# Performance work log

Hardware: AMD Instinct MI355X
Metric: run time of the kernel (lower is better)

The kernel has to match this reference:

```python
import jax, jax.numpy as jnp
import numpy as np

B, CL, TT, D, A, L, G, H = 8, 2048, 1024, 768, 320, 6, 8192, 12
F = 4 * D


def setup_inputs():
    ks = iter(jax.random.split(jax.random.key(0), 80))

    def nrm(shape, std=1.0):
        return jax.random.normal(next(ks), shape, jnp.float32) * std

    sD, sA, sF = 1.0 / np.sqrt(D), 1.0 / np.sqrt(A), 1.0 / np.sqrt(F)
    inp = {
        'context_latents': nrm((B, CL, D)),
        'action_latents': nrm((B, A)),
        'target_indices': jax.random.randint(next(ks), (B, TT), 0, G),
        'ad_w1': nrm((A, D), sA), 'ad_b1': jnp.zeros(D),
        'ad_lnw': jnp.ones(D), 'ad_lnb': jnp.zeros(D),
        'ad_w2': nrm((D, D), sD), 'ad_b2': jnp.zeros(D),
        'mq': nrm((G, D), sD),
        'ln1_w': jnp.ones((L, D)), 'ln1_b': jnp.zeros((L, D)),
        'a_qw': nrm((L, D, D), sD), 'a_qb': jnp.zeros((L, D)),
        'a_kw': nrm((L, D, D), sD), 'a_kb': jnp.zeros((L, D)),
        'a_vw': nrm((L, D, D), sD), 'a_vb': jnp.zeros((L, D)),
        'a_cw': nrm((L, D, D), sD), 'a_cb': jnp.zeros((L, D)),
        'ln2_w': jnp.ones((L, D)), 'ln2_b': jnp.zeros((L, D)),
        's_qw': nrm((L, D, D), sD), 's_qb': jnp.zeros((L, D)),
        's_kw': nrm((L, D, D), sD), 's_kb': jnp.zeros((L, D)),
        's_vw': nrm((L, D, D), sD), 's_vb': jnp.zeros((L, D)),
        's_cw': nrm((L, D, D), sD), 's_cb': jnp.zeros((L, D)),
        'ln3_w': jnp.ones((L, D)), 'ln3_b': jnp.zeros((L, D)),
        'mlp_w1': nrm((L, D, F), sD), 'mlp_b1': jnp.zeros((L, F)),
        'mlp_w2': nrm((L, F, D), sF), 'mlp_b2': jnp.zeros((L, D)),
        'fn_w': jnp.ones(D), 'fn_b': jnp.zeros(D),
        'mu_w': nrm((D, D), sD), 'mu_b': jnp.zeros(D),
        'lv_w': nrm((D, D), sD), 'lv_b': jnp.zeros(D),
    }
    return inp


def _ln(x, w, b, eps=1e-5):
    m = x.mean(-1, keepdims=True)
    v = jnp.var(x, axis=-1, keepdims=True)
    return (x - m) * jax.lax.rsqrt(v + eps) * w + b


def _lin_attn(x, kv, qw, qb, kw, kb, vw, vb, cw, cb):
    # BioLinearAttention: elu(x)+1 feature map, k^T@v reformulation (O(T*hd^2))
    Bq, Tq, Dm = x.shape
    Tk = kv.shape[1]
    hd = Dm // H
    q = (x @ qw + qb).reshape(Bq, Tq, H, hd).transpose(0, 2, 1, 3)
    k = (kv @ kw + kb).reshape(Bq, Tk, H, hd).transpose(0, 2, 1, 3)
    v = (kv @ vw + vb).reshape(Bq, Tk, H, hd).transpose(0, 2, 1, 3)
    q = jax.nn.elu(q) + 1.0
    k = jax.nn.elu(k) + 1.0
    kvm = jnp.einsum('bhkd,bhke->bhde', k, v)  # [B,H,hd,hd]
    ksum = k.sum(axis=2)                        # [B,H,hd]
    z = 1.0 / (jnp.einsum('bhqd,bhd->bhq', q, ksum) + 1e-6)
    y = jnp.einsum('bhqd,bhde->bhqe', q, kvm) * z[..., None]
    y = y.transpose(0, 2, 1, 3).reshape(Bq, Tq, Dm)
    return y @ cw + cb


def reference(context_latents, action_latents, target_indices, ad_w1, ad_b1,
              ad_lnw, ad_lnb, ad_w2, ad_b2, mq, ln1_w, ln1_b, a_qw, a_qb,
              a_kw, a_kb, a_vw, a_vb, a_cw, a_cb, ln2_w, ln2_b, s_qw, s_qb,
              s_kw, s_kb, s_vw, s_vb, s_cw, s_cb, ln3_w, ln3_b, mlp_w1,
              mlp_b1, mlp_w2, mlp_b2, fn_w, fn_b, mu_w, mu_b, lv_w, lv_b):
    # adapter: Linear -> LayerNorm -> GELU(exact) -> Linear
    a = action_latents @ ad_w1 + ad_b1
    a = jax.nn.gelu(_ln(a, ad_lnw, ad_lnb), approximate=False)
    action_emb = (a @ ad_w2 + ad_b2)[:, None, :]  # [B,1,D]
    queries = mq[target_indices]                  # [B,TT,D]
    x = jnp.concatenate([context_latents, queries], axis=1)  # [B,CL+TT,D]
    for i in range(L):
        x = x + _lin_attn(_ln(x, ln1_w[i], ln1_b[i]), action_emb,
                          a_qw[i], a_qb[i], a_kw[i], a_kb[i],
                          a_vw[i], a_vb[i], a_cw[i], a_cb[i])
        xn = _ln(x, ln2_w[i], ln2_b[i])
        x = x + _lin_attn(xn, xn, s_qw[i], s_qb[i], s_kw[i], s_kb[i],
                          s_vw[i], s_vb[i], s_cw[i], s_cb[i])
        h = jax.nn.gelu(_ln(x, ln3_w[i], ln3_b[i]) @ mlp_w1[i] + mlp_b1[i],
                        approximate=True)
        x = x + h @ mlp_w2[i] + mlp_b2[i]
    x = _ln(x, fn_w, fn_b)
    pred = x[:, CL:, :]
    mu = pred @ mu_w + mu_b
    logvar = jnp.clip(pred @ lv_w + lv_b, -10.0, 2.0)
    return mu, logvar
```

## Files before the change

### kernel.cpp

```cpp
#include <hip/hip_runtime.h>
#include <hip/hip_bf16.h>
#include <math.h>

#define B_   8
#define CL_  2048
#define TT_  1024
#define T_   3072
#define D_   768
#define AD_  320
#define L_   6
#define H_   12
#define F_   3072
#define HD_  64
#define BH_  (B_*H_)
#define BT_  (B_*T_)

typedef __bf16 bf16x8 __attribute__((ext_vector_type(8)));
typedef float  f32x4  __attribute__((ext_vector_type(4)));

__device__ __forceinline__ float bf2f(ushort h){
  union { unsigned u; float f; } v; v.u = ((unsigned)h) << 16; return v.f;
}
__device__ __forceinline__ ushort f2bf(float f){
  union { float f; unsigned u; } v; v.f = f;
  unsigned u = v.u;
  return (ushort)((u + 0x7fffu + ((u >> 16) & 1u)) >> 16);
}

__device__ __forceinline__ void gl_lds16(const ushort* g, ushort* l){
  __builtin_amdgcn_global_load_lds((__attribute__((address_space(1))) void*)g,
                                   (__attribute__((address_space(3))) void*)l,
                                   16, 0, 0);
}

__global__ __launch_bounds__(256)
void zero_k(float4* __restrict__ p, int n4)
{
  int i = blockIdx.x*256 + threadIdx.x;
  if (i < n4) p[i] = (float4){0.f,0.f,0.f,0.f};
}

__global__ __launch_bounds__(256)
void tconv_k(const float* __restrict__ in, ushort* __restrict__ out, int K, int N)
{
  __shared__ ushort tile[64*65];
  int n0 = blockIdx.x*64, k0 = blockIdx.y*64;
  int c  = threadIdx.x & 63, rb = threadIdx.x >> 6;
  #pragma unroll
  for (int i = 0; i < 16; i++){
    int r = rb + i*4;
    tile[r*65 + c] = f2bf(in[(size_t)(k0 + r)*N + n0 + c]);
  }
  __syncthreads();
  #pragma unroll
  for (int i = 0; i < 16; i++){
    int r = rb + i*4;
    out[(size_t)(n0 + r)*K + k0 + c] = tile[c*65 + r];
  }
}

template<int EPI>
__global__ __launch_bounds__(256)
void gemm_bf16_k(const ushort* __restrict__ Ag, const ushort* __restrict__ Bt,
                 const float* __restrict__ bias, ushort* __restrict__ outb,
                 float* __restrict__ outf, int N, int K, int lda, int ldb)
{
  __shared__ __align__(16) ushort As[128*64];
  __shared__ __align__(16) ushort Bs[128*64];
  const int tid  = threadIdx.x;
  const int wave = tid >> 6, lane = tid & 63;
  const int q    = lane >> 4, l16 = lane & 15;
  const int bm   = blockIdx.y * 128, bn = blockIdx.x * 128;
  const int wm   = (wave & 1) * 64,  wn = (wave >> 1) * 64;
  const int lr   = lane >> 3;
  const int lc   = ((lane & 7) ^ lr) * 8;

  f32x4 acc[4][4];
  #pragma unroll
  for (int i = 0; i < 4; i++)
    #pragma unroll
    for (int j = 0; j < 4; j++) acc[i][j] = (f32x4){0.f,0.f,0.f,0.f};

  for (int k0 = 0; k0 < K; k0 += 64){
    #pragma unroll
    for (int j = 0; j < 4; j++){
      int r0 = wave*8 + j*32;
      gl_lds16(Ag + (size_t)(bm + r0 + lr)*lda + k0 + lc, As + r0*64);
      gl_lds16(Bt + (size_t)(bn + r0 + lr)*ldb + k0 + lc, Bs + r0*64);
    }
    __syncthreads();
    #pragma unroll
    for (int ks = 0; ks < 2; ks++){
      const int sx = (((ks*4 + q) ^ (l16 & 7)) * 8);
      bf16x8 af[4], bfr[4];
      #pragma unroll
      for (int mt = 0; mt < 4; mt++)
        af[mt]  = *(const bf16x8*)(As + (wm + mt*16 + l16)*64 + sx);
      #pragma unroll
      for (int nt = 0; nt < 4; nt++)
        bfr[nt] = *(const bf16x8*)(Bs + (wn + nt*16 + l16)*64 + sx);
      #pragma unroll
      for (int mt = 0; mt < 4; mt++)
        #pragma unroll
        for (int nt = 0; nt < 4; nt++)
          acc[mt][nt] = __builtin_amdgcn_mfma_f32_16x16x32_bf16(af[mt], bfr[nt], acc[mt][nt], 0, 0, 0);
    }
    __syncthreads();
  }

  #pragma unroll
  for (int nt = 0; nt < 4; nt++){
    int col  = bn + wn + nt*16 + l16;
    float bv = bias ? bias[col] : 0.f;
    #pragma unroll
    for (int mt = 0; mt < 4; mt++){
      #pragma unroll
      for (int r = 0; r < 4; r++){
        int row   = bm + wm + mt*16 + q*4 + r;
        float v   = acc[mt][nt][r] + bv;
        size_t off = (size_t)row*N + col;
        if      (EPI == 0) outb[off] = f2bf(v);
        else if (EPI == 1) outb[off] = f2bf(v > 0.f ? v + 1.f : __expf(v));
        else if (EPI == 2){
          float t = __expf(1.5957691216057308f*v + 0.0713548162726009f*v*v*v);
          outb[off] = f2bf(v - v/(t + 1.f));
        }
        else if (EPI == 3) outf[off] += v;
        else if (EPI == 4) outf[off] = v;
        else if (EPI == 5) outf[off] = fminf(fmaxf(v, -10.f), 2.f);
      }
    }
  }
}

__global__ __launch_bounds__(256)
void y_mfma_k(const ushort* __restrict__ qb, const float* __restrict__ kvm,
              const float* __restrict__ ksum, ushort* __restrict__ yb)
{
  __shared__ __align__(16) ushort Qs[128*72];
  __shared__ __align__(16) ushort Bs[80*72];
  int bh = blockIdx.x, b = bh / H_, h = bh - b*H_;
  int bm = blockIdx.y * 128;
  int tid = threadIdx.x, wave = tid >> 6, lane = tid & 63;
  int q = lane >> 4, l16 = lane & 15;

  const float* kvg = kvm + (size_t)bh*4096;
  #pragma unroll
  for (int rep = 0; rep < 16; rep++){
    int idx = rep*256 + tid;
    int d = idx >> 6, e = idx & 63;
    Bs[e*72 + d] = f2bf(kvg[idx]);
  }
  if (tid < 64) Bs[64*72 + tid] = f2bf(ksum[bh*64 + tid]);
  for (int idx = tid; idx < 15*64; idx += 256){
    int r = 65 + idx/64, c = idx & 63;
    Bs[r*72 + c] = 0;
  }
  const size_t qbase = ((size_t)b*T_ + bm)*D_ + h*HD_;
  #pragma unroll
  for (int i = 0; i < 4; i++){
    int e = i*256 + tid;
    int r = e >> 3, c = (e & 7)*8;
    *(bf16x8*)(Qs + r*72 + c) = *(const bf16x8*)(qb + qbase + (size_t)r*D_ + c);
  }
  __syncthreads();

  int wm = wave*32;
  f32x4 acc[2][5];
  #pragma unroll
  for (int i = 0; i < 2; i++)
    #pragma unroll
    for (int j = 0; j < 5; j++) acc[i][j] = (f32x4){0.f,0.f,0.f,0.f};

  #pragma unroll
  for (int ks = 0; ks < 2; ks++){
    bf16x8 af[2], bfr[5];
    #pragma unroll
    for (int mt = 0; mt < 2; mt++)
      af[mt]  = *(const bf16x8*)(Qs + (wm + mt*16 + l16)*72 + ks*32 + q*8);
    #pragma unroll
    for (int nt = 0; nt < 5; nt++)
      bfr[nt] = *(const bf16x8*)(Bs + (nt*16 + l16)*72 + ks*32 + q*8);
    #pragma unroll
    for (int mt = 0; mt < 2; mt++)
      #pragma unroll
      for (int nt = 0; nt < 5; nt++)
        acc[mt][nt] = __builtin_amdgcn_mfma_f32_16x16x32_bf16(af[mt], bfr[nt], acc[mt][nt], 0, 0, 0);
  }

  #pragma unroll
  for (int mt = 0; mt < 2; mt++){
    #pragma unroll
    for (int r = 0; r < 4; r++){
      float d0 = __shfl(acc[mt][4][r], lane & 48);
      float z  = 1.f / (d0 + 1e-6f);
      int row  = bm + wm + mt*16 + q*4 + r;
      size_t obase = ((size_t)b*T_ + row)*D_ + h*HD_;
      #pragma unroll
      for (int nt = 0; nt < 4; nt++)
        yb[obase + nt*16 + l16] = f2bf(acc[mt][nt][r] * z);
    }
  }
}

__global__ __launch_bounds__(256)
void ln_add_k(float* __restrict__ x, const float* __restrict__ cb,
              const float* __restrict__ w, const float* __restrict__ b,
              ushort* __restrict__ out)
{
  int wave = threadIdx.x >> 6, lane = threadIdx.x & 63;
  int row  = blockIdx.x*4 + wave;
  int bidx = row / T_;
  float* xr = x + (size_t)row*D_;
  const float* cbr = cb + (size_t)bidx*D_;
  float vals[12], s = 0.f, s2 = 0.f;
  #pragma unroll
  for (int j = 0; j < 12; j++){
    int e = j*64 + lane;
    float v = xr[e] + cbr[e];
    xr[e] = v;
    vals[j] = v; s += v; s2 += v*v;
  }
  #pragma unroll
  for (int o = 32; o > 0; o >>= 1){ s += __shfl_xor(s, o); s2 += __shfl_xor(s2, o); }
  float m   = s  * (1.f/768.f);
  float var = s2 * (1.f/768.f) - m*m;
  float rs  = rsqrtf(var + 1e-5f);
  ushort* orow = out + (size_t)row*D_;
  #pragma unroll
  for (int j = 0; j < 12; j++){
    int e = j*64 + lane;
    orow[e] = f2bf((vals[j] - m)*rs*w[e] + b[e]);
  }
}

template<int TAIL>
__global__ __launch_bounds__(256)
void ln_k(const float* __restrict__ x, const float* __restrict__ w,
          const float* __restrict__ b, ushort* __restrict__ out)
{
  int wave = threadIdx.x >> 6, lane = threadIdx.x & 63;
  int row  = blockIdx.x*4 + wave;
  size_t prow;
  if (TAIL){ int bb = row >> 10, t = row & 1023; prow = (size_t)bb*T_ + CL_ + t; }
  else     { prow = row; }
  const float* xr = x + prow*D_;
  float vals[12], s = 0.f, s2 = 0.f;
  #pragma unroll
  for (int j = 0; j < 12; j++){
    float v = xr[j*64 + lane]; vals[j] = v; s += v; s2 += v*v;
  }
  #pragma unroll
  for (int o = 32; o > 0; o >>= 1){ s += __shfl_xor(s, o); s2 += __shfl_xor(s2, o); }
  float m  = s  * (1.f/768.f);
  float var = s2 * (1.f/768.f) - m*m;
  float rs = rsqrtf(var + 1e-5f);
  ushort* orow = out + (size_t)row*D_;
  #pragma unroll
  for (int j = 0; j < 12; j++){
    int e = j*64 + lane;
    orow[e] = f2bf((vals[j] - m)*rs*w[e] + b[e]);
  }
}

__global__ __launch_bounds__(256)
void kvm_k(const ushort* __restrict__ kb, const ushort* __restrict__ vb,
           float* __restrict__ kvm, float* __restrict__ ksum)
{
  __shared__ ushort Ks[32*64], Vs[32*64];
  int bh = blockIdx.x, slice = blockIdx.y;
  int b  = bh / H_, h = bh - b*H_;
  int tid = threadIdx.x;
  int e = tid & 63, dbase = (tid >> 6) * 16;
  float acc[16];
  #pragma unroll
  for (int i = 0; i < 16; i++) acc[i] = 0.f;
  float ksacc = 0.f;
  int r = tid >> 3, c = (tid & 7) * 8;
  const size_t base = (size_t)b*T_*D_ + h*HD_;
  for (int t0 = slice*384; t0 < slice*384 + 384; t0 += 32){
    *(bf16x8*)(Ks + r*64 + c) = *(const bf16x8*)(kb + base + (size_t)(t0 + r)*D_ + c);
    *(bf16x8*)(Vs + r*64 + c) = *(const bf16x8*)(vb + base + (size_t)(t0 + r)*D_ + c);
    __syncthreads();
    #pragma unroll 8
    for (int j = 0; j < 32; j++){
      float vv = bf2f(Vs[j*64 + e]);
      #pragma unroll
      for (int d = 0; d < 16; d++) acc[d] += bf2f(Ks[j*64 + dbase + d]) * vv;
    }
    if (tid < 64){
      #pragma unroll 8
      for (int j = 0; j < 32; j++) ksacc += bf2f(Ks[j*64 + tid]);
    }
    __syncthreads();
  }
  float* kv = kvm + (size_t)bh*4096;
  #pragma unroll
  for (int d = 0; d < 16; d++) atomicAdd(&kv[(dbase + d)*64 + e], acc[d]);
  if (tid < 64) atomicAdd(&ksum[bh*64 + tid], ksacc);
}

__global__ __launch_bounds__(256)
void build_x_k(const float* __restrict__ ctx, const float* __restrict__ mq,
               const int* __restrict__ tgt, float* __restrict__ x)
{
  int idx = blockIdx.x*256 + threadIdx.x;
  int c  = idx % 192;
  int bt = idx / 192;
  int t  = bt % T_, b = bt / T_;
  float4 v;
  if (t < CL_) v = ((const float4*)ctx)[((size_t)b*CL_ + t)*192 + c];
  else {
    int g = tgt[b*TT_ + (t - CL_)];
    v = ((const float4*)mq)[(size_t)g*192 + c];
  }
  ((float4*)x)[idx] = v;
}

__global__ __launch_bounds__(256)
void act1_k(const float* __restrict__ act, const float* __restrict__ w1,
            const float* __restrict__ b1, const float* __restrict__ lnw,
            const float* __restrict__ lnb, float* __restrict__ a1)
{
  __shared__ float buf[768];
  __shared__ float red[256];
  int b = blockIdx.x, tid = threadIdx.x;
  const float* ar = act + b*AD_;
  for (int j = tid; j < 768; j += 256){
    float s = b1[j];
    for (int k = 0; k < AD_; k++) s += ar[k]*w1[k*768 + j];
    buf[j] = s;
  }
  __syncthreads();
  red[tid] = buf[tid] + buf[tid+256] + buf[tid+512];
  __syncthreads();
  for (int o = 128; o > 0; o >>= 1){ if (tid < o) red[tid] += red[tid+o]; __syncthreads(); }
  float m = red[0]*(1.f/768.f);
  __syncthreads();
  float v0 = buf[tid]-m, v1 = buf[tid+256]-m, v2 = buf[tid+512]-m;
  red[tid] = v0*v0 + v1*v1 + v2*v2;
  __syncthreads();
  for (int o = 128; o > 0; o >>= 1){ if (tid < o) red[tid] += red[tid+o]; __syncthreads(); }
  float rs = rsqrtf(red[0]*(1.f/768.f) + 1e-5f);
  __syncthreads();
  for (int j = tid; j < 768; j += 256){
    float v = (buf[j]-m)*rs*lnw[j] + lnb[j];
    a1[b*768 + j] = 0.5f*v*(1.f + erff(v*0.70710678118654752f));
  }
}

__global__ __launch_bounds__(256)
void act2_k(const float* __restrict__ a1, const float* __restrict__ w2,
            const float* __restrict__ b2, float* __restrict__ emb)
{
  __shared__ float inb[768];
  int b = blockIdx.x, tid = threadIdx.x;
  for (int j = tid; j < 768; j += 256) inb[j] = a1[b*768 + j];
  __syncthreads();
  for (int j = tid; j < 768; j += 256){
    float s = b2[j];
    for (int k = 0; k < 768; k++) s += inb[k]*w2[k*768 + j];
    emb[b*768 + j] = s;
  }
}

__global__ __launch_bounds__(256)
void cross_k(const float* __restrict__ emb, const float* __restrict__ vw,
             const float* __restrict__ vbias, const float* __restrict__ cw,
             const float* __restrict__ cbias_in, float* __restrict__ cb_out)
{
  __shared__ float inb[768], tmp[768];
  int b = blockIdx.x, l = blockIdx.y, tid = threadIdx.x;
  const float* wv = vw + (size_t)l*768*768;
  const float* wc = cw + (size_t)l*768*768;
  for (int j = tid; j < 768; j += 256) inb[j] = emb[b*768 + j];
  __syncthreads();
  for (int j = tid; j < 768; j += 256){
    float s = vbias[l*768 + j];
    for (int k = 0; k < 768; k++) s += inb[k]*wv[k*768 + j];
    tmp[j] = s;
  }
  __syncthreads();
  for (int j = tid; j < 768; j += 256){
    float s = cbias_in[l*768 + j];
    for (int k = 0; k < 768; k++) s += tmp[k]*wc[k*768 + j];
    cb_out[((size_t)l*B_ + b)*768 + j] = s;
  }
}

extern "C" void kernel_launch(void* const* d_in, const int* in_sizes, int n_in,
                              void* d_out, int out_size, void* d_ws, size_t ws_size,
                              hipStream_t stream)
{
  (void)in_sizes; (void)n_in; (void)out_size;
  const float* ctx    = (const float*)d_in[0];
  const float* act    = (const float*)d_in[1];
  const int*   tgt    = (const int*)  d_in[2];
  const float* ad_w1  = (const float*)d_in[3];
  const float* ad_b1  = (const float*)d_in[4];
  const float* ad_lnw = (const float*)d_in[5];
  const float* ad_lnb = (const float*)d_in[6];
  const float* ad_w2  = (const float*)d_in[7];
  const float* ad_b2  = (const float*)d_in[8];
  const float* mq     = (const float*)d_in[9];
  const float* a_vw   = (const float*)d_in[16];
  const float* a_vb   = (const float*)d_in[17];
  const float* a_cw   = (const float*)d_in[18];
  const float* a_cb   = (const float*)d_in[19];
  const float* ln2_w  = (const float*)d_in[20];
  const float* ln2_b  = (const float*)d_in[21];
  const float* s_qw   = (const float*)d_in[22];
  const float* s_qb   = (const float*)d_in[23];
  const float* s_kw   = (const float*)d_in[24];
  const float* s_kb   = (const float*)d_in[25];
  const float* s_vw   = (const float*)d_in[26];
  const float* s_vb   = (const float*)d_in[27];
  const float* s_cw   = (const float*)d_in[28];
  const float* s_cb   = (const float*)d_in[29];
  const float* ln3_w  = (const float*)d_in[30];
  const float* ln3_b  = (const float*)d_in[31];
  const float* mlp_w1 = (const float*)d_in[32];
  const float* mlp_b1 = (const float*)d_in[33];
  const float* mlp_w2 = (const float*)d_in[34];
  const float* mlp_b2 = (const float*)d_in[35];
  const float* fn_w   = (const float*)d_in[36];
  const float* fn_b   = (const float*)d_in[37];
  const float* mu_w   = (const float*)d_in[38];
  const float* mu_b   = (const float*)d_in[39];
  const float* lv_w   = (const float*)d_in[40];
  const float* lv_b   = (const float*)d_in[41];

  char* ws = (char*)d_ws;
  size_t off = 0;
  auto alloc = [&](size_t bytes) -> char* {
    char* p = ws + off; off += (bytes + 255) & ~(size_t)255; return p;
  };
  const size_t NTOK = (size_t)BT_;
  float*  x    = (float*) alloc(NTOK*D_*4);
  ushort* xn   = (ushort*)alloc(NTOK*D_*2);
  char*   un   = alloc(3*NTOK*D_*2);
  ushort* qb   = (ushort*)un;
  ushort* kb   = qb + NTOK*D_;
  ushort* vb   = kb + NTOK*D_;
  ushort* hb   = (ushort*)un;
  ushort* wl_sq = (ushort*)alloc((size_t)D_*D_*2);
  ushort* wl_sk = (ushort*)alloc((size_t)D_*D_*2);
  ushort* wl_sv = (ushort*)alloc((size_t)D_*D_*2);
  ushort* wl_sc = (ushort*)alloc((size_t)D_*D_*2);
  ushort* wl_m1 = (ushort*)alloc((size_t)D_*F_*2);
  ushort* wl_m2 = (ushort*)alloc((size_t)F_*D_*2);
  ushort* wt_mu = (ushort*)alloc((size_t)D_*D_*2);
  ushort* wt_lv = (ushort*)alloc((size_t)D_*D_*2);
  float*  kvm   = (float*) alloc((size_t)BH_*HD_*HD_*4);
  float*  ksum  = (float*) alloc((size_t)BH_*HD_*4);
  float*  cbias = (float*) alloc((size_t)L_*B_*D_*4);
  float*  a1    = (float*) alloc((size_t)B_*D_*4);
  float*  emb   = (float*) alloc((size_t)B_*D_*4);

  if (off > ws_size) return;

  dim3 blk(256);

  tconv_k<<<dim3(12,12), blk, 0, stream>>>(mu_w, wt_mu, D_, D_);
  tconv_k<<<dim3(12,12), blk, 0, stream>>>(lv_w, wt_lv, D_, D_);

  act1_k<<<B_, blk, 0, stream>>>(act, ad_w1, ad_b1, ad_lnw, ad_lnb, a1);
  act2_k<<<B_, blk, 0, stream>>>(a1, ad_w2, ad_b2, emb);
  cross_k<<<dim3(B_, L_), blk, 0, stream>>>(emb, a_vw, a_vb, a_cw, a_cb, cbias);

  build_x_k<<<(BT_*192)/256, blk, 0, stream>>>(ctx, mq, tgt, x);

  const int GY = BT_/128;
  const int NZ4 = (BH_*HD_*HD_ + BH_*HD_) / 4;
  for (int i = 0; i < L_; i++){
    tconv_k<<<dim3(12,12), blk, 0, stream>>>(s_qw   + (size_t)i*D_*D_, wl_sq, D_, D_);
    tconv_k<<<dim3(12,12), blk, 0, stream>>>(s_kw   + (size_t)i*D_*D_, wl_sk, D_, D_);
    tconv_k<<<dim3(12,12), blk, 0, stream>>>(s_vw   + (size_t)i*D_*D_, wl_sv, D_, D_);
    tconv_k<<<dim3(12,12), blk, 0, stream>>>(s_cw   + (size_t)i*D_*D_, wl_sc, D_, D_);
    tconv_k<<<dim3(48,12), blk, 0, stream>>>(mlp_w1 + (size_t)i*D_*F_, wl_m1, D_, F_);
    tconv_k<<<dim3(12,48), blk, 0, stream>>>(mlp_w2 + (size_t)i*F_*D_, wl_m2, F_, D_);

    ln_add_k<<<BT_/4, blk, 0, stream>>>(x, cbias + (size_t)i*B_*D_,
                                        ln2_w + i*D_, ln2_b + i*D_, xn);

    gemm_bf16_k<1><<<dim3(6, GY), blk, 0, stream>>>(xn, wl_sq, s_qb + i*D_, qb, nullptr, D_, D_, D_, D_);
    gemm_bf16_k<1><<<dim3(6, GY), blk, 0, stream>>>(xn, wl_sk, s_kb + i*D_, kb, nullptr, D_, D_, D_, D_);
    gemm_bf16_k<0><<<dim3(6, GY), blk, 0, stream>>>(xn, wl_sv, s_vb + i*D_, vb, nullptr, D_, D_, D_, D_);

    zero_k<<<(NZ4 + 255)/256, blk, 0, stream>>>((float4*)kvm, NZ4);
    kvm_k<<<dim3(BH_, 8), blk, 0, stream>>>(kb, vb, kvm, ksum);
    y_mfma_k<<<dim3(BH_, T_/128), blk, 0, stream>>>(qb, kvm, ksum, qb);

    gemm_bf16_k<3><<<dim3(6, GY), blk, 0, stream>>>(qb, wl_sc, s_cb + i*D_, nullptr, x, D_, D_, D_, D_);

    ln_k<0><<<BT_/4, blk, 0, stream>>>(x, ln3_w + i*D_, ln3_b + i*D_, xn);
    for (int c = 0; c < 2; c++){
      gemm_bf16_k<2><<<dim3(12, GY), blk, 0, stream>>>(
          xn, wl_m1 + (size_t)c*1536*D_, mlp_b1 + (size_t)i*F_ + c*1536,
          hb, nullptr, 1536, D_, D_, D_);
      gemm_bf16_k<3><<<dim3(6, GY), blk, 0, stream>>>(
          hb, wl_m2 + (size_t)c*1536, (c == 0) ? (mlp_b2 + (size_t)i*D_) : nullptr,
          nullptr, x, D_, 1536, 1536, F_);
    }
  }

  ln_k<1><<<(B_*TT_)/4, blk, 0, stream>>>(x, fn_w, fn_b, xn);

  float* outmu = (float*)d_out;
  float* outlv = outmu + (size_t)B_*TT_*D_;
  gemm_bf16_k<4><<<dim3(6, (B_*TT_)/128), blk, 0, stream>>>(xn, wt_mu, mu_b, nullptr, outmu, D_, D_, D_, D_);
  gemm_bf16_k<5><<<dim3(6, (B_*TT_)/128), blk, 0, stream>>>(xn, wt_lv, lv_b, nullptr, outlv, D_, D_, D_, D_);
}
```

Baseline: 5.696 ms.

## Batch weight transposes, fuse QKV and mu/logvar GEMMs, split MLP by rows

Merges the four attention-weight transposes into one launch and the two MLP-weight transposes into another. Q, K and V become a single GEMM with N=2304 and a segment-aware epilogue, and the mu and logvar heads become one GEMM. The MLP is now split into two row halves with full F instead of two F-column halves, so W2 is applied once per half with no second accumulate pass. The serial cross-attention constant computation is replaced by parallel atomic-add matvec kernels. These changes reduce launch count and increase per-launch parallelism, but rely on the wl_* and mu/lv weight buffers being contiguous and add atomics and branchy epilogues.

```diff
diff --git a/kernel.cpp b/kernel.cpp
--- a/kernel.cpp
+++ b/kernel.cpp
@@ -40,11 +40,10 @@
   if (i < n4) p[i] = (float4){0.f,0.f,0.f,0.f};
 }
 
-__global__ __launch_bounds__(256)
-void tconv_k(const float* __restrict__ in, ushort* __restrict__ out, int K, int N)
+__device__ __forceinline__ void tconv_body(const float* in, ushort* out,
+                                           int K, int N, int k0, int n0)
 {
   __shared__ ushort tile[64*65];
-  int n0 = blockIdx.x*64, k0 = blockIdx.y*64;
   int c  = threadIdx.x & 63, rb = threadIdx.x >> 6;
   #pragma unroll
   for (int i = 0; i < 16; i++){
@@ -59,10 +58,37 @@
   }
 }
 
+__global__ __launch_bounds__(256)
+void tconv_k(const float* __restrict__ in, ushort* __restrict__ out, int K, int N)
+{
+  tconv_body(in, out, K, N, blockIdx.y*64, blockIdx.x*64);
+}
+
+__global__ __launch_bounds__(256)
+void tconv4_k(const float* __restrict__ s0, const float* __restrict__ s1,
+              const float* __restrict__ s2, const float* __restrict__ s3,
+              ushort* __restrict__ out)
+{
+  int z = blockIdx.z;
+  const float* in = (z == 0) ? s0 : (z == 1) ? s1 : (z == 2) ? s2 : s3;
+  tconv_body(in, out + (size_t)z*D_*D_, D_, D_, blockIdx.y*64, blockIdx.x*64);
+}
+
+__global__ __launch_bounds__(256)
+void tconvM_k(const float* __restrict__ w1, ushort* __restrict__ o1,
+              const float* __restrict__ w2, ushort* __restrict__ o2)
+{
+  if (blockIdx.z == 0)
+    tconv_body(w1, o1, D_, F_, blockIdx.y*64, blockIdx.x*64);
+  else
+    tconv_body(w2, o2, F_, D_, blockIdx.x*64, blockIdx.y*64);
+}
+
 template<int EPI>
 __global__ __launch_bounds__(256)
 void gemm_bf16_k(const ushort* __restrict__ Ag, const ushort* __restrict__ Bt,
-                 const float* __restrict__ bias, ushort* __restrict__ outb,
+                 const float* __restrict__ bias, const float* __restrict__ bias2,
+                 const float* __restrict__ bias3, ushort* __restrict__ outb,
                  float* __restrict__ outf, int N, int K, int lda, int ldb)
 {
   __shared__ __align__(16) ushort As[128*64];
@@ -110,24 +136,40 @@
 
   #pragma unroll
   for (int nt = 0; nt < 4; nt++){
-    int col  = bn + wn + nt*16 + l16;
-    float bv = bias ? bias[col] : 0.f;
+    int col = bn + wn + nt*16 + l16;
+    int seg = 0, cc = col;
+    if (EPI == 6 || EPI == 7){
+      seg = (col >= 1536) ? 2 : (col >= 768) ? 1 : 0;
+      cc  = col - seg*768;
+    }
+    float bv;
+    if      (EPI == 7) bv = (seg == 0) ? bias[cc] : (seg == 1) ? bias2[cc] : bias3[cc];
+    else if (EPI == 6) bv = seg ? bias2[cc] : bias[cc];
+    else               bv = bias ? bias[col] : 0.f;
     #pragma unroll
     for (int mt = 0; mt < 4; mt++){
       #pragma unroll
       for (int r = 0; r < 4; r++){
-        int row   = bm + wm + mt*16 + q*4 + r;
-        float v   = acc[mt][nt][r] + bv;
-        size_t off = (size_t)row*N + col;
-        if      (EPI == 0) outb[off] = f2bf(v);
-        else if (EPI == 1) outb[off] = f2bf(v > 0.f ? v + 1.f : __expf(v));
-        else if (EPI == 2){
-          float t = __expf(1.5957691216057308f*v + 0.0713548162726009f*v*v*v);
-          outb[off] = f2bf(v - v/(t + 1.f));
+        int row = bm + wm + mt*16 + q*4 + r;
+        float v = acc[mt][nt][r] + bv;
+        if (EPI == 7){
+          float o = (seg < 2) ? (v > 0.f ? v + 1.f : __expf(v)) : v;
+          outb[(size_t)seg*((size_t)BT_*D_) + (size_t)row*D_ + cc] = f2bf(o);
+        } else if (EPI == 6){
+          size_t o = (size_t)seg*((size_t)B_*TT_*D_) + (size_t)row*D_ + cc;
+          outf[o] = seg ? fminf(fmaxf(v, -10.f), 2.f) : v;
+        } else {
+          size_t off = (size_t)row*N + col;
+          if      (EPI == 0) outb[off] = f2bf(v);
+          else if (EPI == 1) outb[off] = f2bf(v > 0.f ? v + 1.f : __expf(v));
+          else if (EPI == 2){
+            float t = __expf(1.5957691216057308f*v + 0.0713548162726009f*v*v*v);
+            outb[off] = f2bf(v - v/(t + 1.f));
+          }
+          else if (EPI == 3) outf[off] += v;
+          else if (EPI == 4) outf[off] = v;
+          else if (EPI == 5) outf[off] = fminf(fmaxf(v, -10.f), 2.f);
         }
-        else if (EPI == 3) outf[off] += v;
-        else if (EPI == 4) outf[off] = v;
-        else if (EPI == 5) outf[off] = fminf(fmaxf(v, -10.f), 2.f);
       }
     }
   }
@@ -365,27 +407,41 @@
 }
 
 __global__ __launch_bounds__(256)
-void cross_k(const float* __restrict__ emb, const float* __restrict__ vw,
-             const float* __restrict__ vbias, const float* __restrict__ cw,
-             const float* __restrict__ cbias_in, float* __restrict__ cb_out)
-{
-  __shared__ float inb[768], tmp[768];
-  int b = blockIdx.x, l = blockIdx.y, tid = threadIdx.x;
-  const float* wv = vw + (size_t)l*768*768;
-  const float* wc = cw + (size_t)l*768*768;
-  for (int j = tid; j < 768; j += 256) inb[j] = emb[b*768 + j];
-  __syncthreads();
-  for (int j = tid; j < 768; j += 256){
-    float s = vbias[l*768 + j];
-    for (int k = 0; k < 768; k++) s += inb[k]*wv[k*768 + j];
-    tmp[j] = s;
-  }
-  __syncthreads();
-  for (int j = tid; j < 768; j += 256){
-    float s = cbias_in[l*768 + j];
-    for (int k = 0; k < 768; k++) s += tmp[k]*wc[k*768 + j];
-    cb_out[((size_t)l*B_ + b)*768 + j] = s;
-  }
+void cinit_k(const float* __restrict__ vb, const float* __restrict__ cbv,
+             float* __restrict__ tmp, float* __restrict__ cb)
+{
+  int idx = blockIdx.x*256 + threadIdx.x;
+  int j = idx % 768, l = (idx / 768) / B_;
+  tmp[idx] = vb[l*768 + j];
+  cb[idx]  = cbv[l*768 + j];
+}
+
+template<int IN>
+__global__ __launch_bounds__(256)
+void cmm_k(const float* __restrict__ inp, const float* __restrict__ W,
+           float* __restrict__ out)
+{
+  __shared__ float ein[8*96];
+  int jc = blockIdx.x, kc = blockIdx.y, l = blockIdx.z;
+  int tid = threadIdx.x;
+  int c = tid & 63, ts = tid >> 6;
+  for (int i = tid; i < 768; i += 256){
+    int b = i / 96, kk = i - b*96;
+    ein[i] = IN ? inp[((size_t)l*B_ + b)*768 + kc*96 + kk]
+                : inp[(size_t)b*768 + kc*96 + kk];
+  }
+  __syncthreads();
+  int j = jc*64 + c;
+  const float* w = W + (size_t)l*768*768 + j;
+  float acc[8] = {0,0,0,0,0,0,0,0};
+  for (int kk = ts*24; kk < ts*24 + 24; kk++){
+    float wv = w[(size_t)(kc*96 + kk)*768];
+    #pragma unroll
+    for (int b = 0; b < 8; b++) acc[b] += ein[b*96 + kk] * wv;
+  }
+  #pragma unroll
+  for (int b = 0; b < 8; b++)
+    atomicAdd(&out[((size_t)l*B_ + b)*768 + j], acc[b]);
 }
 
 extern "C" void kernel_launch(void* const* d_in, const int* in_sizes, int n_in,
@@ -454,6 +510,7 @@
   float*  kvm   = (float*) alloc((size_t)BH_*HD_*HD_*4);
   float*  ksum  = (float*) alloc((size_t)BH_*HD_*4);
   float*  cbias = (float*) alloc((size_t)L_*B_*D_*4);
+  float*  ctmp  = (float*) alloc((size_t)L_*B_*D_*4);
   float*  a1    = (float*) alloc((size_t)B_*D_*4);
   float*  emb   = (float*) alloc((size_t)B_*D_*4);
 
@@ -466,48 +523,49 @@
 
   act1_k<<<B_, blk, 0, stream>>>(act, ad_w1, ad_b1, ad_lnw, ad_lnb, a1);
   act2_k<<<B_, blk, 0, stream>>>(a1, ad_w2, ad_b2, emb);
-  cross_k<<<dim3(B_, L_), blk, 0, stream>>>(emb, a_vw, a_vb, a_cw, a_cb, cbias);
+  cinit_k<<<(L_*B_*D_)/256, blk, 0, stream>>>(a_vb, a_cb, ctmp, cbias);
+  cmm_k<0><<<dim3(12,8,L_), blk, 0, stream>>>(emb,  a_vw, ctmp);
+  cmm_k<1><<<dim3(12,8,L_), blk, 0, stream>>>(ctmp, a_cw, cbias);
 
   build_x_k<<<(BT_*192)/256, blk, 0, stream>>>(ctx, mq, tgt, x);
 
   const int GY = BT_/128;
   const int NZ4 = (BH_*HD_*HD_ + BH_*HD_) / 4;
   for (int i = 0; i < L_; i++){
-    tconv_k<<<dim3(12,12), blk, 0, stream>>>(s_qw   + (size_t)i*D_*D_, wl_sq, D_, D_);
-    tconv_k<<<dim3(12,12), blk, 0, stream>>>(s_kw   + (size_t)i*D_*D_, wl_sk, D_, D_);
-    tconv_k<<<dim3(12,12), blk, 0, stream>>>(s_vw   + (size_t)i*D_*D_, wl_sv, D_, D_);
-    tconv_k<<<dim3(12,12), blk, 0, stream>>>(s_cw   + (size_t)i*D_*D_, wl_sc, D_, D_);
-    tconv_k<<<dim3(48,12), blk, 0, stream>>>(mlp_w1 + (size_t)i*D_*F_, wl_m1, D_, F_);
-    tconv_k<<<dim3(12,48), blk, 0, stream>>>(mlp_w2 + (size_t)i*F_*D_, wl_m2, F_, D_);
+    tconv4_k<<<dim3(12,12,4), blk, 0, stream>>>(
+        s_qw + (size_t)i*D_*D_, s_kw + (size_t)i*D_*D_,
+        s_vw + (size_t)i*D_*D_, s_cw + (size_t)i*D_*D_, wl_sq);
+    tconvM_k<<<dim3(48,12,2), blk, 0, stream>>>(
+        mlp_w1 + (size_t)i*D_*F_, wl_m1, mlp_w2 + (size_t)i*F_*D_, wl_m2);
 
     ln_add_k<<<BT_/4, blk, 0, stream>>>(x, cbias + (size_t)i*B_*D_,
                                         ln2_w + i*D_, ln2_b + i*D_, xn);
 
-    gemm_bf16_k<1><<<dim3(6, GY), blk, 0, stream>>>(xn, wl_sq, s_qb + i*D_, qb, nullptr, D_, D_, D_, D_);
-    gemm_bf16_k<1><<<dim3(6, GY), blk, 0, stream>>>(xn, wl_sk, s_kb + i*D_, kb, nullptr, D_, D_, D_, D_);
-    gemm_bf16_k<0><<<dim3(6, GY), blk, 0, stream>>>(xn, wl_sv, s_vb + i*D_, vb, nullptr, D_, D_, D_, D_);
+    gemm_bf16_k<7><<<dim3(18, GY), blk, 0, stream>>>(
+        xn, wl_sq, s_qb + i*D_, s_kb + i*D_, s_vb + i*D_,
+        qb, nullptr, 2304, D_, D_, D_);
 
     zero_k<<<(NZ4 + 255)/256, blk, 0, stream>>>((float4*)kvm, NZ4);
     kvm_k<<<dim3(BH_, 8), blk, 0, stream>>>(kb, vb, kvm, ksum);
     y_mfma_k<<<dim3(BH_, T_/128), blk, 0, stream>>>(qb, kvm, ksum, qb);
 
-    gemm_bf16_k<3><<<dim3(6, GY), blk, 0, stream>>>(qb, wl_sc, s_cb + i*D_, nullptr, x, D_, D_, D_, D_);
+    gemm_bf16_k<3><<<dim3(6, GY), blk, 0, stream>>>(
+        qb, wl_sc, s_cb + i*D_, nullptr, nullptr, nullptr, x, D_, D_, D_, D_);
 
     ln_k<0><<<BT_/4, blk, 0, stream>>>(x, ln3_w + i*D_, ln3_b + i*D_, xn);
-    for (int c = 0; c < 2; c++){
-      gemm_bf16_k<2><<<dim3(12, GY), blk, 0, stream>>>(
-          xn, wl_m1 + (size_t)c*1536*D_, mlp_b1 + (size_t)i*F_ + c*1536,
-          hb, nullptr, 1536, D_, D_, D_);
-      gemm_bf16_k<3><<<dim3(6, GY), blk, 0, stream>>>(
-          hb, wl_m2 + (size_t)c*1536, (c == 0) ? (mlp_b2 + (size_t)i*D_) : nullptr,
-          nullptr, x, D_, 1536, 1536, F_);
+    for (int m = 0; m < 2; m++){
+      const size_t ro = (size_t)m*12288;
+      gemm_bf16_k<2><<<dim3(24, 96), blk, 0, stream>>>(
+          xn + ro*D_, wl_m1, mlp_b1 + (size_t)i*F_, nullptr, nullptr,
+          hb, nullptr, F_, D_, D_, D_);
+      gemm_bf16_k<3><<<dim3(6, 96), blk, 0, stream>>>(
+          hb, wl_m2, mlp_b2 + (size_t)i*D_, nullptr, nullptr,
+          nullptr, x + ro*D_, D_, F_, F_, F_);
     }
   }
 
   ln_k<1><<<(B_*TT_)/4, blk, 0, stream>>>(x, fn_w, fn_b, xn);
 
-  float* outmu = (float*)d_out;
-  float* outlv = outmu + (size_t)B_*TT_*D_;
-  gemm_bf16_k<4><<<dim3(6, (B_*TT_)/128), blk, 0, stream>>>(xn, wt_mu, mu_b, nullptr, outmu, D_, D_, D_, D_);
-  gemm_bf16_k<5><<<dim3(6, (B_*TT_)/128), blk, 0, stream>>>(xn, wt_lv, lv_b, nullptr, outlv, D_, D_, D_, D_);
-}
+  gemm_bf16_k<6><<<dim3(12, (B_*TT_)/128), blk, 0, stream>>>(
+      xn, wt_mu, mu_b, lv_b, nullptr, nullptr, (float*)d_out, 1536, D_, D_, D_);
+}
```

Result: faster. 4.964 ms (-12.8%).
